# Kernel optimization log

Hardware: AMD Instinct MI355X
Metric: run time of the kernel (lower is better)

The kernel has to match this reference:

```python
import jax, jax.numpy as jnp
import numpy as np

N_JOINTS = 21
EDGES = np.array([[0,13],[0,1],[0,4],[0,10],[0,7],[13,14],[14,15],[15,16],[1,2],[2,3],[3,17],[4,5],[5,6],[6,18],[10,11],[11,12],[12,19],[7,8],[8,9],[9,20]], dtype=np.int32)


def _build_adj():
    # SemGCN-style adj_mx_from_edges: symmetric adjacency + self loops, row-normalized
    A = np.zeros((N_JOINTS, N_JOINTS), np.float32)
    A[EDGES[:, 0], EDGES[:, 1]] = 1.0
    A = np.maximum(A, A.T)
    A = A + np.eye(N_JOINTS, dtype=np.float32)
    A = A / A.sum(axis=1, keepdims=True)
    return A


def setup_inputs() -> dict:
    key = jax.random.key(0)
    ks = jax.random.split(key, 8)
    B, C, Hm, Wm = 128, 235, 64, 64
    heads, fo = 4, 32
    feature_s = jax.random.normal(ks[0], (B, C, Hm, Wm), jnp.float32)
    target_s = jax.random.uniform(ks[1], (B, N_JOINTS, Hm, Wm), jnp.float32)
    bn_gamma = jnp.ones((N_JOINTS,), jnp.float32)
    bn_beta = jnp.zeros((N_JOINTS,), jnp.float32)
    gat_w = jax.random.normal(ks[2], (C, heads * fo), jnp.float32) * 0.05
    gat_att_src = jax.random.normal(ks[3], (heads, fo), jnp.float32) * 0.1
    gat_att_dst = jax.random.normal(ks[4], (heads, fo), jnp.float32) * 0.1
    gat_bias = jnp.zeros((heads * fo,), jnp.float32)
    cheb_w = jax.random.normal(ks[5], (2, heads * fo, 3), jnp.float32) * 0.05
    cheb_bias = jnp.zeros((3,), jnp.float32)
    # PyG GATConv adds self loops: 20 skeleton edges + 21 self edges = 41
    src = np.concatenate([EDGES[:, 0], np.arange(N_JOINTS, dtype=np.int32)])
    dst = np.concatenate([EDGES[:, 1], np.arange(N_JOINTS, dtype=np.int32)])
    return {
        'feature_s': feature_s, 'target_s': target_s,
        'bn_gamma': bn_gamma, 'bn_beta': bn_beta,
        'gat_w': gat_w, 'gat_att_src': gat_att_src, 'gat_att_dst': gat_att_dst,
        'gat_bias': gat_bias, 'cheb_w': cheb_w, 'cheb_bias': cheb_bias,
        'adj': jnp.asarray(_build_adj()),
        'edge_src': jnp.asarray(src), 'edge_dst': jnp.asarray(dst),
    }


def reference(feature_s, target_s, bn_gamma, bn_beta, gat_w, gat_att_src, gat_att_dst, gat_bias, cheb_w, cheb_bias, adj, edge_src, edge_dst):
    B, C = feature_s.shape[0], feature_s.shape[1]
    N = target_s.shape[1]
    # per-sample query embedding: [B, 21, HW] @ [B, HW, C] -> [B, 21, C]
    f = feature_s.reshape(B, C, -1)
    t = target_s.reshape(B, N, -1)
    q = jnp.einsum('bnp,bcp->bnc', t, f)
    # BatchNorm1d(21), training mode: normalize per joint-channel over (B, C)
    mean = q.mean(axis=(0, 2), keepdims=True)
    var = q.var(axis=(0, 2), keepdims=True)
    q = (q - mean) * jax.lax.rsqrt(var + 1e-5) * bn_gamma[None, :, None] + bn_beta[None, :, None]
    q = jnp.where(q >= 0, q, 0.1 * q)  # LeakyReLU(0.1)
    # GATConv (4 heads, 32 dims, concat) vmapped over batch of identical graphs
    heads, fo = gat_att_src.shape
    h = (q @ gat_w).reshape(B, N, heads, fo)
    a_src = jnp.einsum('bnhf,hf->bnh', h, gat_att_src)
    a_dst = jnp.einsum('bnhf,hf->bnh', h, gat_att_dst)
    e = a_src[:, edge_src] + a_dst[:, edge_dst]           # [B, E, H]
    e = jnp.where(e >= 0, e, 0.2 * e)                     # GAT default negative_slope=0.2
    seg_max = jax.vmap(lambda v: jax.ops.segment_max(v, edge_dst, num_segments=N))
    seg_sum = jax.vmap(lambda v: jax.ops.segment_sum(v, edge_dst, num_segments=N))
    m = seg_max(e)                                        # [B, N, H]
    ex = jnp.exp(e - m[:, edge_dst])
    den = seg_sum(ex)
    alpha = ex / den[:, edge_dst]                         # per-dst softmax
    msg = alpha[..., None] * h[:, edge_src]               # [B, E, H, Fo]
    out = seg_sum(msg.reshape(B, -1, heads * fo))         # [B, N, H*Fo]
    x = out + gat_bias
    # ChebConv K=2 (GraFormer-style): T0 = I, T1 = L = I - D^{-1/2} A D^{-1/2}
    d = jnp.sum(adj, axis=-1) ** -0.5
    L = jnp.eye(N, dtype=adj.dtype) - d[:, None] * adj * d[None, :]
    y = jnp.einsum('bnc,co->bno', x, cheb_w[0]) + jnp.einsum('mn,bnc,co->bmo', L, x, cheb_w[1])
    return y + cheb_bias
```

## Files before the change

kernel.cpp:

```cpp
#include <hip/hip_runtime.h>
#include <hip/hip_bf16.h>

constexpr int B  = 128;
constexpr int C  = 235;
constexpr int N  = 21;
constexpr int HW = 4096;
constexpr int HO = 128;
constexpr int E  = 41;

typedef __attribute__((ext_vector_type(8)))  short  short8;
typedef __attribute__((ext_vector_type(16))) float  f32x16;

__device__ inline unsigned short bf16r(float x) {
    return __bfloat16_as_ushort(__float2bfloat16(x));
}

constexpr int KSPLIT = 8;
constexpr int KRANGE = HW / KSPLIT;
constexpr int NSLOT  = KSPLIT;

__global__ __launch_bounds__(256) void k1_qgemm(
    const float* __restrict__ f,
    const float* __restrict__ t,
    float* __restrict__ qp)
{
    const int j = blockIdx.x;
    const int logical = (j & 7) * 256 + (j >> 3);
    const int cg = logical & 1;
    const int ks = (logical >> 1) & 7;
    const int b  = logical >> 4;

    const int tid  = threadIdx.x;
    const int wave = tid >> 6;
    const int lane = tid & 63;
    const int l31  = lane & 31;
    const int kh   = lane >> 5;

    const float* fb = f + (size_t)b * C * HW;
    const float* tb = t + (size_t)b * N * HW;

    const int arow = (l31 < N) ? l31 : (N - 1);
    const int col  = cg * 128 + wave * 32 + l31;
    const int colc = (col < C) ? col : (C - 1);

    const float* pa = tb + (size_t)arow * HW + kh * 8;
    const float* pb = fb + (size_t)colc * HW + kh * 8;

    f32x16 acc = {};
    const int kbase = ks * KRANGE;
    const int kend  = kbase + KRANGE;

    float4 A0 = *reinterpret_cast<const float4*>(pa + kbase);
    float4 A1 = *reinterpret_cast<const float4*>(pa + kbase + 4);
    float4 B0 = *reinterpret_cast<const float4*>(pb + kbase);
    float4 B1 = *reinterpret_cast<const float4*>(pb + kbase + 4);

    #pragma unroll 4
    for (int k = kbase; k < kend; k += 16) {
        const float4 a0 = A0, a1 = A1, b0 = B0, b1 = B1;
        if (k + 16 < kend) {
            A0 = *reinterpret_cast<const float4*>(pa + k + 16);
            A1 = *reinterpret_cast<const float4*>(pa + k + 20);
            B0 = *reinterpret_cast<const float4*>(pb + k + 16);
            B1 = *reinterpret_cast<const float4*>(pb + k + 20);
        }
        union { short8 v; unsigned short u[8]; } av, bv;
        av.u[0] = bf16r(a0.x); av.u[1] = bf16r(a0.y);
        av.u[2] = bf16r(a0.z); av.u[3] = bf16r(a0.w);
        av.u[4] = bf16r(a1.x); av.u[5] = bf16r(a1.y);
        av.u[6] = bf16r(a1.z); av.u[7] = bf16r(a1.w);
        bv.u[0] = bf16r(b0.x); bv.u[1] = bf16r(b0.y);
        bv.u[2] = bf16r(b0.z); bv.u[3] = bf16r(b0.w);
        bv.u[4] = bf16r(b1.x); bv.u[5] = bf16r(b1.y);
        bv.u[6] = bf16r(b1.z); bv.u[7] = bf16r(b1.w);
        acc = __builtin_amdgcn_mfma_f32_32x32x16_bf16(av.v, bv.v, acc, 0, 0, 0);
    }

    float* qpk = qp + ((size_t)ks * B + b) * N * C;
    #pragma unroll
    for (int reg = 0; reg < 16; reg++) {
        const int row = (reg & 3) + 8 * (reg >> 2) + 4 * kh;
        if (row < N && col < C)
            qpk[row * C + col] = acc[reg];
    }
}

__global__ __launch_bounds__(256) void k1b_bn(
    const float* __restrict__ qp,
    float* __restrict__ q,
    float* __restrict__ bnp)
{
    const int b    = blockIdx.x;
    const int tid  = threadIdx.x;
    const int wave = tid >> 6;
    const int lane = tid & 63;
    __shared__ float rs[N][4], rs2[N][4];
    constexpr int S = B * N * C;

    for (int n = 0; n < N; ++n) {
        float v = 0.f;
        const int idx = (b * N + n) * C + tid;
        if (tid < C) {
            #pragma unroll
            for (int p = 0; p < NSLOT; p++) v += qp[(size_t)p * S + idx];
            q[idx] = v;
        }
        float s = v, s2 = v * v;
        for (int off = 32; off; off >>= 1) {
            s  += __shfl_down(s,  off);
            s2 += __shfl_down(s2, off);
        }
        if (lane == 0) { rs[n][wave] = s; rs2[n][wave] = s2; }
    }
    __syncthreads();
    if (tid < N) {
        const float S1 = rs[tid][0] + rs[tid][1] + rs[tid][2] + rs[tid][3];
        const float S2 = rs2[tid][0] + rs2[tid][1] + rs2[tid][2] + rs2[tid][3];
        bnp[(b * N + tid) * 2]     = S1;
        bnp[(b * N + tid) * 2 + 1] = S2;
    }
}

__global__ __launch_bounds__(256) void k3_tail(
    const float* __restrict__ q,
    const float* __restrict__ bnp,
    const float* __restrict__ gamma,
    const float* __restrict__ beta,
    const float* __restrict__ gatw,
    const float* __restrict__ attsrc,
    const float* __restrict__ attdst,
    const float* __restrict__ gatbias,
    const float* __restrict__ chebw,
    const float* __restrict__ chebbias,
    const float* __restrict__ adj,
    const int* __restrict__ esrc,
    const int* __restrict__ edst,
    float* __restrict__ out)
{
    __shared__ float ql[N][C + 1];
    __shared__ float Wl[48][HO];
    __shared__ float hl[N][HO];
    __shared__ float xl[N][HO];
    __shared__ float stl[N][2];
    __shared__ float asrcl[N][4], adstl[N][4];
    __shared__ float el[E][4], alphal[E][4];
    __shared__ float mx[N][4], den[N][4];
    __shared__ float zl[N][3], t0l[N][3], dsl[N];
    __shared__ int esl[E], edl[E];

    const int b = blockIdx.x;
    const int tid = threadIdx.x;

    if (tid < N) {
        float S1 = 0.f, S2 = 0.f;
        for (int bb = 0; bb < B; bb++) {
            S1 += bnp[(bb * N + tid) * 2];
            S2 += bnp[(bb * N + tid) * 2 + 1];
        }
        const float cnt  = (float)(B * C);
        const float mean = S1 / cnt;
        const float var  = S2 / cnt - mean * mean;
        const float sc   = gamma[tid] * rsqrtf(var + 1e-5f);
        stl[tid][0] = sc;
        stl[tid][1] = beta[tid] - mean * sc;
    }
    if (tid < E) { esl[tid] = esrc[tid]; edl[tid] = edst[tid]; }
    __syncthreads();

    for (int v = tid; v < N * C; v += 256) {
        const int n = v / C, c = v % C;
        float x = q[((size_t)b * N + n) * C + c];
        x = x * stl[n][0] + stl[n][1];
        ql[n][c] = (x >= 0.f) ? x : 0.1f * x;
    }
    for (int v = tid; v < N * HO; v += 256) hl[v >> 7][v & 127] = 0.f;
    __syncthreads();

    for (int k0 = 0; k0 < C; k0 += 48) {
        const int kc = (C - k0) < 48 ? (C - k0) : 48;
        for (int v = tid; v < kc * HO; v += 256) {
            const int kk = v >> 7, o = v & 127;
            Wl[kk][o] = gatw[(size_t)(k0 + kk) * HO + o];
        }
        __syncthreads();
        for (int idx = tid; idx < N * HO; idx += 256) {
            const int n = idx >> 7, o = idx & 127;
            float s = hl[n][o];
            for (int kk = 0; kk < kc; kk++)
                s += ql[n][k0 + kk] * Wl[kk][o];
            hl[n][o] = s;
        }
        __syncthreads();
    }

    if (tid < N * 4) {
        const int n = tid >> 2, h = tid & 3;
        float ss = 0.f, sd = 0.f;
        for (int fo = 0; fo < 32; fo++) {
            const float hv = hl[n][h * 32 + fo];
            ss += hv * attsrc[h * 32 + fo];
            sd += hv * attdst[h * 32 + fo];
        }
        asrcl[n][h] = ss; adstl[n][h] = sd;
    }
    __syncthreads();
    if (tid < E * 4) {
        const int e = tid >> 2, h = tid & 3;
        const float v = asrcl[esl[e]][h] + adstl[edl[e]][h];
        el[e][h] = (v >= 0.f) ? v : 0.2f * v;
    }
    __syncthreads();
    if (tid < N * 4) {
        const int n = tid >> 2, h = tid & 3;
        float m = -1e30f;
        for (int e = 0; e < E; e++)
            if (edl[e] == n) m = fmaxf(m, el[e][h]);
        mx[n][h] = m;
    }
    __syncthreads();
    if (tid < E * 4) {
        const int e = tid >> 2, h = tid & 3;
        el[e][h] = __expf(el[e][h] - mx[edl[e]][h]);
    }
    __syncthreads();
    if (tid < N * 4) {
        const int n = tid >> 2, h = tid & 3;
        float s = 0.f;
        for (int e = 0; e < E; e++)
            if (edl[e] == n) s += el[e][h];
        den[n][h] = s;
    }
    __syncthreads();
    if (tid < E * 4) {
        const int e = tid >> 2, h = tid & 3;
        alphal[e][h] = el[e][h] / den[edl[e]][h];
    }
    __syncthreads();

    for (int idx = tid; idx < N * HO; idx += 256) {
        const int n = idx >> 7, o = idx & 127, h = o >> 5;
        float s = 0.f;
        for (int e = 0; e < E; e++)
            if (edl[e] == n) s += alphal[e][h] * hl[esl[e]][o];
        xl[n][o] = s + gatbias[o];
    }
    if (tid < N) {
        float s = 0.f;
        for (int j2 = 0; j2 < N; j2++) s += adj[tid * N + j2];
        dsl[tid] = rsqrtf(s);
    }
    __syncthreads();

    if (tid < N * 3) {
        const int n = tid / 3, o = tid % 3;
        float s0 = 0.f, sz = 0.f;
        for (int c2 = 0; c2 < HO; c2++) {
            const float xv = xl[n][c2];
            s0 += xv * chebw[(size_t)c2 * 3 + o];
            sz += xv * chebw[(size_t)(HO + c2) * 3 + o];
        }
        t0l[n][o] = s0; zl[n][o] = sz;
    }
    __syncthreads();
    if (tid < N * 3) {
        const int m = tid / 3, o = tid % 3;
        float s = t0l[m][o] + zl[m][o];
        for (int n2 = 0; n2 < N; n2++)
            s -= dsl[m] * adj[m * N + n2] * dsl[n2] * zl[n2][o];
        out[(size_t)b * N * 3 + tid] = s + chebbias[o];
    }
}

extern "C" void kernel_launch(void* const* d_in, const int* in_sizes, int n_in,
                              void* d_out, int out_size, void* d_ws, size_t ws_size,
                              hipStream_t stream) {
    const float* feature  = (const float*)d_in[0];
    const float* target   = (const float*)d_in[1];
    const float* gamma    = (const float*)d_in[2];
    const float* beta     = (const float*)d_in[3];
    const float* gatw     = (const float*)d_in[4];
    const float* attsrc   = (const float*)d_in[5];
    const float* attdst   = (const float*)d_in[6];
    const float* gatbias  = (const float*)d_in[7];
    const float* chebw    = (const float*)d_in[8];
    const float* chebbias = (const float*)d_in[9];
    const float* adj      = (const float*)d_in[10];
    const int*   esrc     = (const int*)d_in[11];
    const int*   edst     = (const int*)d_in[12];

    constexpr int QS = B * N * C;
    float* qp  = (float*)d_ws;
    float* q   = qp + (size_t)NSLOT * QS;
    float* bnp = q + QS;
    float* out = (float*)d_out;

    hipLaunchKernelGGL(k1_qgemm, dim3(2 * KSPLIT * B), dim3(256), 0, stream,
                       feature, target, qp);
    hipLaunchKernelGGL(k1b_bn, dim3(B), dim3(256), 0, stream, qp, q, bnp);
    hipLaunchKernelGGL(k3_tail, dim3(B), dim3(256), 0, stream,
                       q, bnp, gamma, beta, gatw, attsrc, attdst, gatbias,
                       chebw, chebbias, adj, esrc, edst, out);
}
```

Before: 224.2 us.

## Give each GEMM wave two column tiles and parallelize BN stat reduction

The batched q GEMM now launches one block per (k-split, batch) on a 2D grid. Each wave computes two 32-column MFMA tiles, so one A fragment load feeds two MFMAs and the separate column-group blocks go away. Feature loads use nontemporal hints, and the explicit register prefetch and block-index swizzle are removed. The BN partial sums are stored joint-major, and the tail kernel reduces them with 12 threads per joint plus a shared-memory combine instead of a serial 128-iteration loop per joint. This halves the block count and drops the prefetch, which may reduce latency hiding for a kernel dominated by streaming reads.

```diff
diff --git a/kernel.cpp b/kernel.cpp
--- a/kernel.cpp
+++ b/kernel.cpp
@@ -10,9 +10,15 @@
 
 typedef __attribute__((ext_vector_type(8)))  short  short8;
 typedef __attribute__((ext_vector_type(16))) float  f32x16;
+typedef __attribute__((ext_vector_type(4)))  float  f32x4;
 
 __device__ inline unsigned short bf16r(float x) {
     return __bfloat16_as_ushort(__float2bfloat16(x));
+}
+
+__device__ inline f32x4 ntload4(const float* p) {
+    const f32x4* p4 = reinterpret_cast<const f32x4*>(p);
+    return __builtin_nontemporal_load(p4);
 }
 
 constexpr int KSPLIT = 8;
@@ -24,12 +30,8 @@
     const float* __restrict__ t,
     float* __restrict__ qp)
 {
-    const int j = blockIdx.x;
-    const int logical = (j & 7) * 256 + (j >> 3);
-    const int cg = logical & 1;
-    const int ks = (logical >> 1) & 7;
-    const int b  = logical >> 4;
-
+    const int b    = blockIdx.y;
+    const int ks   = blockIdx.x;
     const int tid  = threadIdx.x;
     const int wave = tid >> 6;
     const int lane = tid & 63;
@@ -40,48 +42,54 @@
     const float* tb = t + (size_t)b * N * HW;
 
     const int arow = (l31 < N) ? l31 : (N - 1);
-    const int col  = cg * 128 + wave * 32 + l31;
-    const int colc = (col < C) ? col : (C - 1);
+    const int c1   = wave * 64 + l31;
+    const int c2   = wave * 64 + 32 + l31;
+    const int c1c  = (c1 < C) ? c1 : (C - 1);
+    const int c2c  = (c2 < C) ? c2 : (C - 1);
 
     const float* pa = tb + (size_t)arow * HW + kh * 8;
-    const float* pb = fb + (size_t)colc * HW + kh * 8;
-
-    f32x16 acc = {};
-    const int kbase = ks * KRANGE;
-    const int kend  = kbase + KRANGE;
-
-    float4 A0 = *reinterpret_cast<const float4*>(pa + kbase);
-    float4 A1 = *reinterpret_cast<const float4*>(pa + kbase + 4);
-    float4 B0 = *reinterpret_cast<const float4*>(pb + kbase);
-    float4 B1 = *reinterpret_cast<const float4*>(pb + kbase + 4);
-
-    #pragma unroll 4
-    for (int k = kbase; k < kend; k += 16) {
-        const float4 a0 = A0, a1 = A1, b0 = B0, b1 = B1;
-        if (k + 16 < kend) {
-            A0 = *reinterpret_cast<const float4*>(pa + k + 16);
-            A1 = *reinterpret_cast<const float4*>(pa + k + 20);
-            B0 = *reinterpret_cast<const float4*>(pb + k + 16);
-            B1 = *reinterpret_cast<const float4*>(pb + k + 20);
-        }
-        union { short8 v; unsigned short u[8]; } av, bv;
-        av.u[0] = bf16r(a0.x); av.u[1] = bf16r(a0.y);
-        av.u[2] = bf16r(a0.z); av.u[3] = bf16r(a0.w);
-        av.u[4] = bf16r(a1.x); av.u[5] = bf16r(a1.y);
-        av.u[6] = bf16r(a1.z); av.u[7] = bf16r(a1.w);
-        bv.u[0] = bf16r(b0.x); bv.u[1] = bf16r(b0.y);
-        bv.u[2] = bf16r(b0.z); bv.u[3] = bf16r(b0.w);
-        bv.u[4] = bf16r(b1.x); bv.u[5] = bf16r(b1.y);
-        bv.u[6] = bf16r(b1.z); bv.u[7] = bf16r(b1.w);
-        acc = __builtin_amdgcn_mfma_f32_32x32x16_bf16(av.v, bv.v, acc, 0, 0, 0);
+    const float* p1 = fb + (size_t)c1c  * HW + kh * 8;
+    const float* p2 = fb + (size_t)c2c  * HW + kh * 8;
+
+    f32x16 acc0 = {};
+    f32x16 acc1 = {};
+
+    const int kend = ks * KRANGE + KRANGE;
+    #pragma unroll 2
+    for (int k = ks * KRANGE; k < kend; k += 16) {
+        const float4 alo = *reinterpret_cast<const float4*>(pa + k);
+        const float4 ahi = *reinterpret_cast<const float4*>(pa + k + 4);
+        const f32x4 b1l = ntload4(p1 + k);
+        const f32x4 b1h = ntload4(p1 + k + 4);
+        const f32x4 b2l = ntload4(p2 + k);
+        const f32x4 b2h = ntload4(p2 + k + 4);
+
+        union { short8 v; unsigned short u[8]; } av, bv1, bv2;
+        av.u[0]  = bf16r(alo.x); av.u[1]  = bf16r(alo.y);
+        av.u[2]  = bf16r(alo.z); av.u[3]  = bf16r(alo.w);
+        av.u[4]  = bf16r(ahi.x); av.u[5]  = bf16r(ahi.y);
+        av.u[6]  = bf16r(ahi.z); av.u[7]  = bf16r(ahi.w);
+        bv1.u[0] = bf16r(b1l[0]); bv1.u[1] = bf16r(b1l[1]);
+        bv1.u[2] = bf16r(b1l[2]); bv1.u[3] = bf16r(b1l[3]);
+        bv1.u[4] = bf16r(b1h[0]); bv1.u[5] = bf16r(b1h[1]);
+        bv1.u[6] = bf16r(b1h[2]); bv1.u[7] = bf16r(b1h[3]);
+        bv2.u[0] = bf16r(b2l[0]); bv2.u[1] = bf16r(b2l[1]);
+        bv2.u[2] = bf16r(b2l[2]); bv2.u[3] = bf16r(b2l[3]);
+        bv2.u[4] = bf16r(b2h[0]); bv2.u[5] = bf16r(b2h[1]);
+        bv2.u[6] = bf16r(b2h[2]); bv2.u[7] = bf16r(b2h[3]);
+
+        acc0 = __builtin_amdgcn_mfma_f32_32x32x16_bf16(av.v, bv1.v, acc0, 0, 0, 0);
+        acc1 = __builtin_amdgcn_mfma_f32_32x32x16_bf16(av.v, bv2.v, acc1, 0, 0, 0);
     }
 
     float* qpk = qp + ((size_t)ks * B + b) * N * C;
     #pragma unroll
     for (int reg = 0; reg < 16; reg++) {
         const int row = (reg & 3) + 8 * (reg >> 2) + 4 * kh;
-        if (row < N && col < C)
-            qpk[row * C + col] = acc[reg];
+        if (row < N) {
+            if (c1 < C) qpk[row * C + c1] = acc0[reg];
+            if (c2 < C) qpk[row * C + c2] = acc1[reg];
+        }
     }
 }
 
@@ -116,8 +124,8 @@
     if (tid < N) {
         const float S1 = rs[tid][0] + rs[tid][1] + rs[tid][2] + rs[tid][3];
         const float S2 = rs2[tid][0] + rs2[tid][1] + rs2[tid][2] + rs2[tid][3];
-        bnp[(b * N + tid) * 2]     = S1;
-        bnp[(b * N + tid) * 2 + 1] = S2;
+        bnp[(tid * B + b) * 2]     = S1;
+        bnp[(tid * B + b) * 2 + 1] = S2;
     }
 }
 
@@ -151,18 +159,28 @@
     const int b = blockIdx.x;
     const int tid = threadIdx.x;
 
-    if (tid < N) {
+    {
+        const int n = tid / 12, sub = tid % 12;
         float S1 = 0.f, S2 = 0.f;
-        for (int bb = 0; bb < B; bb++) {
-            S1 += bnp[(bb * N + tid) * 2];
-            S2 += bnp[(bb * N + tid) * 2 + 1];
-        }
-        const float cnt  = (float)(B * C);
-        const float mean = S1 / cnt;
-        const float var  = S2 / cnt - mean * mean;
-        const float sc   = gamma[tid] * rsqrtf(var + 1e-5f);
-        stl[tid][0] = sc;
-        stl[tid][1] = beta[tid] - mean * sc;
+        if (n < N) {
+            for (int bb = sub; bb < B; bb += 12) {
+                S1 += bnp[(n * B + bb) * 2];
+                S2 += bnp[(n * B + bb) * 2 + 1];
+            }
+        }
+        __shared__ float g1[N][12], g2[N][12];
+        if (n < N) { g1[n][sub] = S1; g2[n][sub] = S2; }
+        __syncthreads();
+        if (tid < N) {
+            float a1 = 0.f, a2 = 0.f;
+            for (int s = 0; s < 12; s++) { a1 += g1[tid][s]; a2 += g2[tid][s]; }
+            const float cnt  = (float)(B * C);
+            const float mean = a1 / cnt;
+            const float var  = a2 / cnt - mean * mean;
+            const float sc   = gamma[tid] * rsqrtf(var + 1e-5f);
+            stl[tid][0] = sc;
+            stl[tid][1] = beta[tid] - mean * sc;
+        }
     }
     if (tid < E) { esl[tid] = esrc[tid]; edl[tid] = edst[tid]; }
     __syncthreads();
@@ -294,7 +312,7 @@
     float* bnp = q + QS;
     float* out = (float*)d_out;
 
-    hipLaunchKernelGGL(k1_qgemm, dim3(2 * KSPLIT * B), dim3(256), 0, stream,
+    hipLaunchKernelGGL(k1_qgemm, dim3(KSPLIT, B), dim3(256), 0, stream,
                        feature, target, qp);
     hipLaunchKernelGGL(k1b_bn, dim3(B), dim3(256), 0, stream, qp, q, bnp);
     hipLaunchKernelGGL(k3_tail, dim3(B), dim3(256), 0, stream,
```

Measured after the change: 265.8 us. +18.6%, slower.
